# Optimization experiments

Hardware: AMD Instinct MI355X
Metric: run time of the kernel (lower is better)

The kernel has to match this reference:

```python
import jax, jax.numpy as jnp
import numpy as np

L, E, D = 4, 512, 256   # layers, model dim (=2*D bidirectional), per-direction hidden
T, B = 100, 1000
EPS = 1e-5

def _layernorm(x, g, b):
    m = x.mean(-1, keepdims=True)
    v = x.var(-1, keepdims=True)
    return (x - m) / jnp.sqrt(v + EPS) * g + b

def _dir_scan(U, vf, vr, bf, br):
    # U: (T, B, 4, D) pre-projected gates; SRU elementwise recurrence over time.
    def step(c, u):
        f = jax.nn.sigmoid(u[:, 1] + vf * c + bf)
        c2 = f * c + (1.0 - f) * u[:, 0]
        r = jax.nn.sigmoid(u[:, 2] + vr * c2 + br)
        h = r * c2 + (1.0 - r) * u[:, 3]   # highway with projected residual u3
        return c2, h
    c0 = jnp.zeros((U.shape[1], U.shape[-1]), U.dtype)
    _, H = jax.lax.scan(step, c0, U)
    return H

def setup_inputs() -> dict:
    key = jax.random.key(0)
    ks = jax.random.split(key, 6)
    return {
        "sentence": jax.random.normal(ks[0], (T, B, E), jnp.float32),
        "sru_W": jax.random.normal(ks[1], (L, 2, E, 4 * D), jnp.float32) / np.float32(np.sqrt(E)),
        "sru_v": jax.random.normal(ks[2], (L, 2, 2, D), jnp.float32) * 0.05,
        "sru_b": jnp.zeros((L, 2, 2, D), jnp.float32),
        "ln_g": jnp.ones((L, E), jnp.float32),
        "ln_b": jnp.zeros((L, E), jnp.float32),
        "W1": jax.random.normal(ks[3], (E, E), jnp.float32) / np.float32(np.sqrt(E)),
        "b1": jnp.zeros((E,), jnp.float32),
        "bn_g": jnp.ones((E,), jnp.float32),
        "bn_b": jnp.zeros((E,), jnp.float32),
        "bn_mean": jnp.zeros((E,), jnp.float32),
        "bn_var": jnp.ones((E,), jnp.float32),
        "W2": jax.random.normal(ks[4], (E, 4), jnp.float32) / np.float32(np.sqrt(E)),
        "b2": jnp.zeros((4,), jnp.float32),
    }

def reference(sentence, sru_W, sru_v, sru_b, ln_g, ln_b, W1, b1, bn_g, bn_b, bn_mean, bn_var, W2, b2):
    x = sentence  # (T, B, E)
    for l in range(L):
        xl = _layernorm(x, ln_g[l], ln_b[l])
        # batched projection for both directions: (2, T, B, 4, D)
        U = jnp.einsum('tbi,dik->dtbk', xl, sru_W[l]).reshape(2, T, B, 4, D)
        Hf = _dir_scan(U[0], sru_v[l, 0, 0], sru_v[l, 0, 1], sru_b[l, 0, 0], sru_b[l, 0, 1])
        Hb = _dir_scan(U[1][::-1], sru_v[l, 1, 0], sru_v[l, 1, 1], sru_b[l, 1, 0], sru_b[l, 1, 1])[::-1]
        x = jnp.concatenate([Hf, Hb], axis=-1)  # (T, B, E)
    # head on flattened tokens (eval mode: dropout off, BN uses running stats)
    h = x.reshape(-1, E) @ W1 + b1
    h = (h - bn_mean) / jnp.sqrt(bn_var + EPS) * bn_g + bn_b
    h = jax.nn.relu(h)
    logits = h @ W2 + b2  # (T*B, 4)
    return jax.nn.log_softmax(logits, axis=-1)
```

## Files before the change

kernel.cpp:

```cpp
#include <hip/hip_runtime.h>
#include <stdint.h>

#define T_DIM 100
#define B_DIM 1000
#define E_DIM 512
#define D_DIM 256
#define L_DIM 4
#define M_TOK (T_DIM * B_DIM)
#define M_PAD 100096
#define K_DIM 512

typedef unsigned short u16;
typedef __bf16 bf16x8 __attribute__((ext_vector_type(8)));
typedef float f32x4 __attribute__((ext_vector_type(4)));
typedef unsigned short ushort8 __attribute__((ext_vector_type(8)));

__device__ __forceinline__ u16 f2bf(float f) {
  unsigned int u = __builtin_bit_cast(unsigned int, f);
  u += 0x7fffu + ((u >> 16) & 1u);
  return (u16)(u >> 16);
}
__device__ __forceinline__ float bf2f(u16 h) {
  unsigned int u = ((unsigned int)h) << 16;
  return __builtin_bit_cast(float, u);
}

__device__ __forceinline__ void gld16(const u16* g, u16* l) {
  __builtin_amdgcn_global_load_lds(
      (const __attribute__((address_space(1))) unsigned int*)g,
      (__attribute__((address_space(3))) unsigned int*)l, 16, 0, 0);
}

__global__ void transpose_cast(const float* __restrict__ in, u16* __restrict__ out,
                               int R, int C) {
  __shared__ float t[32][33];
  const int s = blockIdx.z;
  const float* ib = in + (size_t)s * R * C;
  u16* ob = out + (size_t)s * R * C;
  const int c0 = blockIdx.x * 32, r0 = blockIdx.y * 32;
  const int tx = threadIdx.x, ty = threadIdx.y;
#pragma unroll
  for (int j = 0; j < 4; ++j)
    t[ty + j * 8][tx] = ib[(size_t)(r0 + ty + j * 8) * C + c0 + tx];
  __syncthreads();
#pragma unroll
  for (int j = 0; j < 4; ++j)
    ob[(size_t)(c0 + ty + j * 8) * R + r0 + tx] = f2bf(t[tx][ty + j * 8]);
}

__global__ __launch_bounds__(256) void ln_cast_kernel(
    const float* __restrict__ x, const float* __restrict__ g,
    const float* __restrict__ b, u16* __restrict__ out) {
  const int wid = threadIdx.x >> 6, lane = threadIdx.x & 63;
  const int row = blockIdx.x * 4 + wid;
  u16* orow = out + (size_t)row * E_DIM + lane * 8;
  if (row >= M_TOK) {
    ushort8 z = {0, 0, 0, 0, 0, 0, 0, 0};
    *(ushort8*)orow = z;
    return;
  }
  const float* xr = x + (size_t)row * E_DIM + lane * 8;
  const float4 a = *(const float4*)xr;
  const float4 c = *(const float4*)(xr + 4);
  float xe[8] = {a.x, a.y, a.z, a.w, c.x, c.y, c.z, c.w};
  float s = 0.f, q = 0.f;
#pragma unroll
  for (int u = 0; u < 8; ++u) { s += xe[u]; q += xe[u] * xe[u]; }
#pragma unroll
  for (int off = 32; off; off >>= 1) {
    s += __shfl_xor(s, off, 64);
    q += __shfl_xor(q, off, 64);
  }
  const float mean = s * (1.0f / 512.0f);
  const float var = q * (1.0f / 512.0f) - mean * mean;
  const float rstd = rsqrtf(var + 1e-5f);
  const float4 g0 = *(const float4*)(g + lane * 8);
  const float4 g1 = *(const float4*)(g + lane * 8 + 4);
  const float4 b0 = *(const float4*)(b + lane * 8);
  const float4 b1v = *(const float4*)(b + lane * 8 + 4);
  float ge[8] = {g0.x, g0.y, g0.z, g0.w, g1.x, g1.y, g1.z, g1.w};
  float be[8] = {b0.x, b0.y, b0.z, b0.w, b1v.x, b1v.y, b1v.z, b1v.w};
  ushort8 o;
#pragma unroll
  for (int u = 0; u < 8; ++u)
    o[u] = f2bf((xe[u] - mean) * rstd * ge[u] + be[u]);
  *(ushort8*)orow = o;
}

__global__ __launch_bounds__(256) void cast_kernel(const float* __restrict__ x,
                                                   u16* __restrict__ out) {
  const size_t idx = (size_t)blockIdx.x * 256 + threadIdx.x;
  const size_t e0 = idx * 8;
  const size_t row = e0 >> 9;
  ushort8 o;
  if (row >= M_TOK) {
    ushort8 z = {0, 0, 0, 0, 0, 0, 0, 0};
    o = z;
  } else {
    const float4 a = *(const float4*)(x + e0);
    const float4 c = *(const float4*)(x + e0 + 4);
    o[0] = f2bf(a.x); o[1] = f2bf(a.y); o[2] = f2bf(a.z); o[3] = f2bf(a.w);
    o[4] = f2bf(c.x); o[5] = f2bf(c.y); o[6] = f2bf(c.z); o[7] = f2bf(c.w);
  }
  *(ushort8*)(out + e0) = o;
}

__global__ __launch_bounds__(256, 2) void gemm_bf16(
    const u16* __restrict__ A, const u16* __restrict__ B, u16* __restrict__ C,
    int N) {
  __shared__ u16 As[128 * 32];
  __shared__ u16 Bs[128 * 32];
  const int tid = threadIdx.x;
  const int wave = tid >> 6, lane = tid & 63;
  const int wm = wave >> 1, wn = wave & 1;
  const size_t m0 = (size_t)blockIdx.x * 128;
  const int n0 = blockIdx.y * 128;
  const int z = blockIdx.z;

  const u16* Ag = A + (m0 + wave * 32 + (lane >> 2)) * K_DIM + (lane & 3) * 8;
  const u16* Bg = B + ((size_t)z * N + n0 + wave * 32 + (lane >> 2)) * K_DIM +
                  (lane & 3) * 8;
  u16* Al = As + wave * 1024;
  u16* Bl = Bs + wave * 1024;

  f32x4 acc[4][4] = {};
  const int rA = lane & 15;
  const int ko = (lane >> 4) * 8;

  for (int kt = 0; kt < K_DIM; kt += 32) {
    gld16(Ag + kt, Al);
    gld16(Ag + kt + 16 * K_DIM, Al + 512);
    gld16(Bg + kt, Bl);
    gld16(Bg + kt + 16 * K_DIM, Bl + 512);
    __syncthreads();

    bf16x8 af[4], bfr[4];
#pragma unroll
    for (int mi = 0; mi < 4; ++mi)
      af[mi] = *(const bf16x8*)&As[(wm * 64 + mi * 16 + rA) * 32 + ko];
#pragma unroll
    for (int ni = 0; ni < 4; ++ni)
      bfr[ni] = *(const bf16x8*)&Bs[(wn * 64 + ni * 16 + rA) * 32 + ko];
#pragma unroll
    for (int mi = 0; mi < 4; ++mi)
#pragma unroll
      for (int ni = 0; ni < 4; ++ni)
        acc[mi][ni] = __builtin_amdgcn_mfma_f32_16x16x32_bf16(
            af[mi], bfr[ni], acc[mi][ni], 0, 0, 0);
    __syncthreads();
  }

  u16* Cb = C + (size_t)z * M_PAD * N;
  const int rr = (lane >> 4) * 4;
  const int cc = lane & 15;
#pragma unroll
  for (int mi = 0; mi < 4; ++mi) {
#pragma unroll
    for (int ni = 0; ni < 4; ++ni) {
      const size_t row = m0 + wm * 64 + mi * 16 + rr;
      const int col = n0 + wn * 64 + ni * 16 + cc;
#pragma unroll
      for (int r = 0; r < 4; ++r)
        Cb[(row + r) * N + col] = f2bf(acc[mi][ni][r]);
    }
  }
}

__global__ __launch_bounds__(256) void sru_scan(const u16* __restrict__ U,
                                                const float* __restrict__ v,
                                                const float* __restrict__ bb,
                                                float* __restrict__ xout) {
  const int d = threadIdx.x;
  const int b = blockIdx.x;
  const int dir = blockIdx.y;
  const float vf = v[(dir * 2 + 0) * 256 + d];
  const float vr = v[(dir * 2 + 1) * 256 + d];
  const float bf = bb[(dir * 2 + 0) * 256 + d];
  const float br = bb[(dir * 2 + 1) * 256 + d];
  const u16* Ud = U + (size_t)dir * M_PAD * 1024;
  float c = 0.f;
  for (int s = 0; s < T_DIM; ++s) {
    const int t = dir ? (T_DIM - 1 - s) : s;
    const size_t base = ((size_t)t * B_DIM + b) * 1024 + d;
    const float u0 = bf2f(Ud[base]);
    const float u1 = bf2f(Ud[base + 256]);
    const float u2 = bf2f(Ud[base + 512]);
    const float u3 = bf2f(Ud[base + 768]);
    const float f = 1.f / (1.f + __expf(-(u1 + vf * c + bf)));
    c = f * c + (1.f - f) * u0;
    const float r = 1.f / (1.f + __expf(-(u2 + vr * c + br)));
    const float h = r * c + (1.f - r) * u3;
    xout[((size_t)t * B_DIM + b) * 512 + dir * 256 + d] = h;
  }
}

__global__ __launch_bounds__(256) void head_kernel(
    const u16* __restrict__ h, const float* __restrict__ b1,
    const float* __restrict__ bn_g, const float* __restrict__ bn_b,
    const float* __restrict__ bn_mean, const float* __restrict__ bn_var,
    const float* __restrict__ W2, const float* __restrict__ b2,
    float* __restrict__ out) {
  const int wid = threadIdx.x >> 6, lane = threadIdx.x & 63;
  const int row = blockIdx.x * 4 + wid;
  const u16* hr = h + (size_t)row * E_DIM + lane * 8;
  const ushort8 hv = *(const ushort8*)hr;
  float s0 = 0.f, s1 = 0.f, s2 = 0.f, s3 = 0.f;
  const int j0 = lane * 8;
#pragma unroll
  for (int u = 0; u < 8; ++u) {
    const int j = j0 + u;
    const float hb = bf2f(hv[u]) + b1[j];
    float hn = (hb - bn_mean[j]) * rsqrtf(bn_var[j] + 1e-5f) * bn_g[j] + bn_b[j];
    hn = fmaxf(hn, 0.f);
    const float4 w = *(const float4*)(W2 + j * 4);
    s0 += hn * w.x; s1 += hn * w.y; s2 += hn * w.z; s3 += hn * w.w;
  }
#pragma unroll
  for (int off = 32; off; off >>= 1) {
    s0 += __shfl_xor(s0, off, 64);
    s1 += __shfl_xor(s1, off, 64);
    s2 += __shfl_xor(s2, off, 64);
    s3 += __shfl_xor(s3, off, 64);
  }
  if (lane == 0) {
    const float4 bv = *(const float4*)b2;
    const float l0 = s0 + bv.x, l1 = s1 + bv.y, l2 = s2 + bv.z, l3 = s3 + bv.w;
    const float mx = fmaxf(fmaxf(l0, l1), fmaxf(l2, l3));
    const float lse =
        mx + logf(__expf(l0 - mx) + __expf(l1 - mx) + __expf(l2 - mx) + __expf(l3 - mx));
    float4 o = {l0 - lse, l1 - lse, l2 - lse, l3 - lse};
    *(float4*)(out + (size_t)row * 4) = o;
  }
}

extern "C" void kernel_launch(void* const* d_in, const int* in_sizes, int n_in,
                              void* d_out, int out_size, void* d_ws, size_t ws_size,
                              hipStream_t stream) {
  const float* sentence = (const float*)d_in[0];
  const float* sru_W = (const float*)d_in[1];
  const float* sru_v = (const float*)d_in[2];
  const float* sru_b = (const float*)d_in[3];
  const float* ln_g = (const float*)d_in[4];
  const float* ln_b = (const float*)d_in[5];
  const float* W1 = (const float*)d_in[6];
  const float* b1 = (const float*)d_in[7];
  const float* bn_g = (const float*)d_in[8];
  const float* bn_b = (const float*)d_in[9];
  const float* bn_mean = (const float*)d_in[10];
  const float* bn_var = (const float*)d_in[11];
  const float* W2 = (const float*)d_in[12];
  const float* b2 = (const float*)d_in[13];

  char* ws = (char*)d_ws;
  const size_t X_OFF = 0;
  const size_t XL_OFF = X_OFF + (size_t)M_TOK * 512 * 4;
  const size_t U_OFF = XL_OFF + (size_t)M_PAD * 512 * 2;
  const size_t WT_OFF = U_OFF + (size_t)2 * M_PAD * 1024 * 2;
  const size_t W1T_OFF = WT_OFF + (size_t)8 * 512 * 1024 * 2;
  float* x_buf = (float*)(ws + X_OFF);
  u16* xl = (u16*)(ws + XL_OFF);
  u16* U = (u16*)(ws + U_OFF);
  u16* WT = (u16*)(ws + WT_OFF);
  u16* W1T = (u16*)(ws + W1T_OFF);
  u16* hbuf = U;

  transpose_cast<<<dim3(32, 16, 8), dim3(32, 8), 0, stream>>>(sru_W, WT, 512, 1024);
  transpose_cast<<<dim3(16, 16, 1), dim3(32, 8), 0, stream>>>(W1, W1T, 512, 512);

  for (int l = 0; l < L_DIM; ++l) {
    const float* xin = (l == 0) ? sentence : x_buf;
    ln_cast_kernel<<<M_PAD / 4, 256, 0, stream>>>(xin, ln_g + l * 512,
                                                  ln_b + l * 512, xl);
    gemm_bf16<<<dim3(M_PAD / 128, 1024 / 128, 2), 256, 0, stream>>>(
        xl, WT + (size_t)l * 2 * 1024 * 512, U, 1024);
    sru_scan<<<dim3(1000, 2), 256, 0, stream>>>(U, sru_v + l * 1024,
                                                sru_b + l * 1024, x_buf);
  }
  cast_kernel<<<M_PAD * 512 / 8 / 256, 256, 0, stream>>>(x_buf, xl);
  gemm_bf16<<<dim3(M_PAD / 128, 512 / 128, 1), 256, 0, stream>>>(xl, W1T, hbuf, 512);
  head_kernel<<<M_TOK / 4, 256, 0, stream>>>(hbuf, b1, bn_g, bn_b, bn_mean,
                                             bn_var, W2, b2, (float*)d_out);
}
```

Measured before the change: 2.430 ms.

## Store SRU hidden states in bf16, swizzle GEMM LDS, reorder grid, drop cast pass

```diff
diff --git a/kernel.cpp b/kernel.cpp
--- a/kernel.cpp
+++ b/kernel.cpp
@@ -48,21 +48,31 @@
     ob[(size_t)(c0 + ty + j * 8) * R + r0 + tx] = f2bf(t[tx][ty + j * 8]);
 }
 
+__global__ __launch_bounds__(256) void zero_pad(u16* __restrict__ xl) {
+  const int i = blockIdx.x * 256 + threadIdx.x;
+  ushort8 z = {0, 0, 0, 0, 0, 0, 0, 0};
+  *(ushort8*)(xl + (size_t)M_TOK * 512 + (size_t)i * 8) = z;
+}
+
+template <typename TI>
 __global__ __launch_bounds__(256) void ln_cast_kernel(
-    const float* __restrict__ x, const float* __restrict__ g,
+    const TI* __restrict__ x, const float* __restrict__ g,
     const float* __restrict__ b, u16* __restrict__ out) {
   const int wid = threadIdx.x >> 6, lane = threadIdx.x & 63;
   const int row = blockIdx.x * 4 + wid;
-  u16* orow = out + (size_t)row * E_DIM + lane * 8;
-  if (row >= M_TOK) {
-    ushort8 z = {0, 0, 0, 0, 0, 0, 0, 0};
-    *(ushort8*)orow = z;
-    return;
-  }
-  const float* xr = x + (size_t)row * E_DIM + lane * 8;
-  const float4 a = *(const float4*)xr;
-  const float4 c = *(const float4*)(xr + 4);
-  float xe[8] = {a.x, a.y, a.z, a.w, c.x, c.y, c.z, c.w};
+  float xe[8];
+  if constexpr (sizeof(TI) == 4) {
+    const float* xr = (const float*)x + (size_t)row * E_DIM + lane * 8;
+    const float4 a = *(const float4*)xr;
+    const float4 c = *(const float4*)(xr + 4);
+    xe[0] = a.x; xe[1] = a.y; xe[2] = a.z; xe[3] = a.w;
+    xe[4] = c.x; xe[5] = c.y; xe[6] = c.z; xe[7] = c.w;
+  } else {
+    const u16* xr = (const u16*)x + (size_t)row * E_DIM + lane * 8;
+    const ushort8 hv = *(const ushort8*)xr;
+#pragma unroll
+    for (int u = 0; u < 8; ++u) xe[u] = bf2f(hv[u]);
+  }
   float s = 0.f, q = 0.f;
 #pragma unroll
   for (int u = 0; u < 8; ++u) { s += xe[u]; q += xe[u] * xe[u]; }
@@ -84,48 +94,33 @@
 #pragma unroll
   for (int u = 0; u < 8; ++u)
     o[u] = f2bf((xe[u] - mean) * rstd * ge[u] + be[u]);
-  *(ushort8*)orow = o;
-}
-
-__global__ __launch_bounds__(256) void cast_kernel(const float* __restrict__ x,
-                                                   u16* __restrict__ out) {
-  const size_t idx = (size_t)blockIdx.x * 256 + threadIdx.x;
-  const size_t e0 = idx * 8;
-  const size_t row = e0 >> 9;
-  ushort8 o;
-  if (row >= M_TOK) {
-    ushort8 z = {0, 0, 0, 0, 0, 0, 0, 0};
-    o = z;
-  } else {
-    const float4 a = *(const float4*)(x + e0);
-    const float4 c = *(const float4*)(x + e0 + 4);
-    o[0] = f2bf(a.x); o[1] = f2bf(a.y); o[2] = f2bf(a.z); o[3] = f2bf(a.w);
-    o[4] = f2bf(c.x); o[5] = f2bf(c.y); o[6] = f2bf(c.z); o[7] = f2bf(c.w);
-  }
-  *(ushort8*)(out + e0) = o;
-}
-
-__global__ __launch_bounds__(256, 2) void gemm_bf16(
+  *(ushort8*)(out + (size_t)row * E_DIM + lane * 8) = o;
+}
+
+__global__ __launch_bounds__(256, 4) void gemm_bf16(
     const u16* __restrict__ A, const u16* __restrict__ B, u16* __restrict__ C,
-    int N) {
+    int N, int ntil_shift) {
   __shared__ u16 As[128 * 32];
   __shared__ u16 Bs[128 * 32];
   const int tid = threadIdx.x;
   const int wave = tid >> 6, lane = tid & 63;
   const int wm = wave >> 1, wn = wave & 1;
-  const size_t m0 = (size_t)blockIdx.x * 128;
-  const int n0 = blockIdx.y * 128;
-  const int z = blockIdx.z;
-
-  const u16* Ag = A + (m0 + wave * 32 + (lane >> 2)) * K_DIM + (lane & 3) * 8;
+  const int nz = blockIdx.x;
+  const int z = nz >> ntil_shift;
+  const int n0 = (nz & ((1 << ntil_shift) - 1)) << 7;
+  const size_t m0 = (size_t)blockIdx.y * 128;
+
+  const int c_ld = (lane & 3) ^ ((lane >> 3) & 3);
+  const u16* Ag = A + (m0 + wave * 32 + (lane >> 2)) * K_DIM + c_ld * 8;
   const u16* Bg = B + ((size_t)z * N + n0 + wave * 32 + (lane >> 2)) * K_DIM +
-                  (lane & 3) * 8;
+                  c_ld * 8;
   u16* Al = As + wave * 1024;
   u16* Bl = Bs + wave * 1024;
 
   f32x4 acc[4][4] = {};
   const int rA = lane & 15;
-  const int ko = (lane >> 4) * 8;
+  const int ch = lane >> 4;
+  const int sw = (ch ^ ((rA >> 1) & 3)) * 8;
 
   for (int kt = 0; kt < K_DIM; kt += 32) {
     gld16(Ag + kt, Al);
@@ -137,10 +132,10 @@
     bf16x8 af[4], bfr[4];
 #pragma unroll
     for (int mi = 0; mi < 4; ++mi)
-      af[mi] = *(const bf16x8*)&As[(wm * 64 + mi * 16 + rA) * 32 + ko];
+      af[mi] = *(const bf16x8*)&As[(wm * 64 + mi * 16 + rA) * 32 + sw];
 #pragma unroll
     for (int ni = 0; ni < 4; ++ni)
-      bfr[ni] = *(const bf16x8*)&Bs[(wn * 64 + ni * 16 + rA) * 32 + ko];
+      bfr[ni] = *(const bf16x8*)&Bs[(wn * 64 + ni * 16 + rA) * 32 + sw];
 #pragma unroll
     for (int mi = 0; mi < 4; ++mi)
 #pragma unroll
@@ -169,7 +164,7 @@
 __global__ __launch_bounds__(256) void sru_scan(const u16* __restrict__ U,
                                                 const float* __restrict__ v,
                                                 const float* __restrict__ bb,
-                                                float* __restrict__ xout) {
+                                                u16* __restrict__ xout) {
   const int d = threadIdx.x;
   const int b = blockIdx.x;
   const int dir = blockIdx.y;
@@ -190,7 +185,7 @@
     c = f * c + (1.f - f) * u0;
     const float r = 1.f / (1.f + __expf(-(u2 + vr * c + br)));
     const float h = r * c + (1.f - r) * u3;
-    xout[((size_t)t * B_DIM + b) * 512 + dir * 256 + d] = h;
+    xout[((size_t)t * B_DIM + b) * 512 + dir * 256 + d] = f2bf(h);
   }
 }
 
@@ -252,13 +247,13 @@
   const float* b2 = (const float*)d_in[13];
 
   char* ws = (char*)d_ws;
-  const size_t X_OFF = 0;
-  const size_t XL_OFF = X_OFF + (size_t)M_TOK * 512 * 4;
-  const size_t U_OFF = XL_OFF + (size_t)M_PAD * 512 * 2;
+  const size_t XL_OFF = 0;
+  const size_t X_OFF = XL_OFF + (size_t)M_PAD * 512 * 2;
+  const size_t U_OFF = X_OFF + (size_t)M_TOK * 512 * 2;
   const size_t WT_OFF = U_OFF + (size_t)2 * M_PAD * 1024 * 2;
   const size_t W1T_OFF = WT_OFF + (size_t)8 * 512 * 1024 * 2;
-  float* x_buf = (float*)(ws + X_OFF);
   u16* xl = (u16*)(ws + XL_OFF);
+  u16* x_buf = (u16*)(ws + X_OFF);
   u16* U = (u16*)(ws + U_OFF);
   u16* WT = (u16*)(ws + WT_OFF);
   u16* W1T = (u16*)(ws + W1T_OFF);
@@ -266,18 +261,22 @@
 
   transpose_cast<<<dim3(32, 16, 8), dim3(32, 8), 0, stream>>>(sru_W, WT, 512, 1024);
   transpose_cast<<<dim3(16, 16, 1), dim3(32, 8), 0, stream>>>(W1, W1T, 512, 512);
+  zero_pad<<<24, 256, 0, stream>>>(xl);
 
   for (int l = 0; l < L_DIM; ++l) {
-    const float* xin = (l == 0) ? sentence : x_buf;
-    ln_cast_kernel<<<M_PAD / 4, 256, 0, stream>>>(xin, ln_g + l * 512,
-                                                  ln_b + l * 512, xl);
-    gemm_bf16<<<dim3(M_PAD / 128, 1024 / 128, 2), 256, 0, stream>>>(
-        xl, WT + (size_t)l * 2 * 1024 * 512, U, 1024);
+    if (l == 0)
+      ln_cast_kernel<float><<<M_TOK / 4, 256, 0, stream>>>(
+          sentence, ln_g, ln_b, xl);
+    else
+      ln_cast_kernel<u16><<<M_TOK / 4, 256, 0, stream>>>(
+          x_buf, ln_g + l * 512, ln_b + l * 512, xl);
+    gemm_bf16<<<dim3(16, M_PAD / 128), 256, 0, stream>>>(
+        xl, WT + (size_t)l * 2 * 1024 * 512, U, 1024, 3);
+    u16* xo = (l == L_DIM - 1) ? xl : x_buf;
     sru_scan<<<dim3(1000, 2), 256, 0, stream>>>(U, sru_v + l * 1024,
-                                                sru_b + l * 1024, x_buf);
-  }
-  cast_kernel<<<M_PAD * 512 / 8 / 256, 256, 0, stream>>>(x_buf, xl);
-  gemm_bf16<<<dim3(M_PAD / 128, 512 / 128, 1), 256, 0, stream>>>(xl, W1T, hbuf, 512);
+                                                sru_b + l * 1024, xo);
+  }
+  gemm_bf16<<<dim3(4, M_PAD / 128), 256, 0, stream>>>(xl, W1T, hbuf, 512, 2);
   head_kernel<<<M_TOK / 4, 256, 0, stream>>>(hbuf, b1, bn_g, bn_b, bn_mean,
                                              bn_var, W2, b2, (float*)d_out);
 }
```

Result: faster. 2.220 ms (-8.6%).
